# Kernel optimization log

Hardware: AMD Instinct MI355X
Metric: run time of the kernel (lower is better)

## Reference

```python
import jax, jax.numpy as jnp
import numpy as np

GRID_SIZE = 5
ORDER = 3  # spline_order
H_STEP = 2.0 / GRID_SIZE  # grid_range = [-1, 1]
GRID = jnp.arange(-ORDER, GRID_SIZE + ORDER + 1, dtype=jnp.float32) * H_STEP - 1.0  # (12,)


def b_splines(x):
    # x: (N, F) -> bases: (N, F, GRID_SIZE + ORDER) via Cox-de Boor recursion
    g = GRID
    xx = x[..., None]
    bases = ((xx >= g[:-1]) & (xx < g[1:])).astype(x.dtype)
    for k in range(1, ORDER + 1):
        left = (xx - g[:-(k + 1)]) / (g[k:-1] - g[:-(k + 1)]) * bases[..., :-1]
        right = (g[k + 1:] - xx) / (g[k + 1:] - g[1:-k]) * bases[..., 1:]
        bases = left + right
    return bases


def kan_linear(x, bw, sw, sc):
    # x: (N, F); bw: (O, F); sw: (O, F, C); sc: (O, F)
    base = jax.nn.silu(x) @ bw.T
    spline = jnp.einsum('nfc,ofc->no', b_splines(x), sw * sc[..., None])
    return base + spline


def kan_conv(x, bw, sw, sc):
    # x: (B, C, H, W); 3x3 patches, padding 1, stride 1 -> KANLinear over C*9 features
    B, C, H, W = x.shape
    patches = jax.lax.conv_general_dilated_patches(x, (3, 3), (1, 1), ((1, 1), (1, 1)))  # (B, C*9, H, W)
    p = patches.transpose(0, 2, 3, 1).reshape(B * H * W, C * 9)
    o = kan_linear(p, bw, sw, sc)  # (B*H*W, Cout)
    return o.reshape(B, H, W, -1).transpose(0, 3, 1, 2)


def maxpool2(x):
    B, C, H, W = x.shape
    return x.reshape(B, C, H // 2, 2, W // 2, 2).max(axis=(3, 5))


def setup_inputs() -> dict:
    key = jax.random.key(0)
    ks = jax.random.split(key, 32)
    d = {}
    d['x'] = jax.random.normal(ks[0], (128, 3, 32, 32), dtype=jnp.float32)
    conv_specs = [(3, 4), (4, 8), (8, 16), (16, 32)]
    i = 1
    for li, (cin, cout) in enumerate(conv_specs, 1):
        fin = cin * 9
        d[f'bw{li}'] = jax.random.normal(ks[i], (cout, fin), dtype=jnp.float32) * (1.0 / np.sqrt(fin)); i += 1
        d[f'sw{li}'] = jax.random.normal(ks[i], (cout, fin, GRID_SIZE + ORDER), dtype=jnp.float32) * 0.1; i += 1
        d[f'sc{li}'] = jax.random.normal(ks[i], (cout, fin), dtype=jnp.float32) * (1.0 / np.sqrt(fin)); i += 1
    lin_specs = [(2048, 2048), (1024, 2048), (10, 1024)]
    for li, (o, inn) in enumerate(lin_specs, 1):
        d[f'w{li}'] = jax.random.normal(ks[i], (o, inn), dtype=jnp.float32) * (1.0 / np.sqrt(inn)); i += 1
        d[f'b{li}'] = jnp.zeros((o,), dtype=jnp.float32); i += 1
    return d


def reference(x, bw1, sw1, sc1, bw2, sw2, sc2, bw3, sw3, sc3, bw4, sw4, sc4, w1, b1, w2, b2, w3, b3):
    x = kan_conv(x, bw1, sw1, sc1)
    x = kan_conv(x, bw2, sw2, sc2)
    x = maxpool2(x)
    x = kan_conv(x, bw3, sw3, sc3)
    x = kan_conv(x, bw4, sw4, sc4)
    x = maxpool2(x)
    x = x.reshape(x.shape[0], -1)  # (B, 32*8*8)
    x = jax.nn.relu(x @ w1.T + b1)
    x = jax.nn.relu(x @ w2.T + b2)
    return x @ w3.T + b3
```

## Files before the change

### kernel.cpp

```cpp
#include <hip/hip_runtime.h>

#define BATCH 128
#define AST 88

typedef __attribute__((ext_vector_type(8))) short bf16x8;
typedef __attribute__((ext_vector_type(16))) float f32x16;

__device__ __forceinline__ void spline_acts(float xv, float act[9]) {
    act[0] = xv * (1.0f / (1.0f + __expf(-xv)));
    float g[12];
#pragma unroll
    for (int i = 0; i < 12; ++i) g[i] = (float)(i - 3) * 0.4f - 1.0f;
    float bb[11];
#pragma unroll
    for (int c = 0; c < 11; ++c) bb[c] = (xv >= g[c] && xv < g[c + 1]) ? 1.0f : 0.0f;
#pragma unroll
    for (int k = 1; k <= 3; ++k) {
#pragma unroll
        for (int c = 0; c + k < 11; ++c) {
            float left  = (xv - g[c]) * (1.0f / (g[c + k] - g[c])) * bb[c];
            float right = (g[c + k + 1] - xv) * (1.0f / (g[c + k + 1] - g[c + 1])) * bb[c + 1];
            bb[c] = left + right;
        }
    }
#pragma unroll
    for (int c = 0; c < 8; ++c) act[c + 1] = bb[c];
}

__device__ __constant__ float ZPAD[9] = {0.0f, 0.0f, 0.0f, 0.02083333333f,
                                         0.47916666667f, 0.47916666667f,
                                         0.02083333333f, 0.0f, 0.0f};

__device__ __forceinline__ void bf16split(float x, ushort& h, ushort& l) {
    union { float f; unsigned u; } a; a.f = x;
    unsigned r = a.u + 0x7FFF + ((a.u >> 16) & 1);
    h = (ushort)(r >> 16);
    union { unsigned u; float f; } hf; hf.u = (unsigned)h << 16;
    union { float f; unsigned u; } bres; bres.f = x - hf.f;
    unsigned r2 = bres.u + 0x7FFF + ((bres.u >> 16) & 1);
    l = (ushort)(r2 >> 16);
}

__device__ __forceinline__ float wval(const float* bw, const float* sw, const float* sc,
                                      int F, int f, int j, int o) {
    if (j == 0) return bw[o * F + f];
    return sw[(o * F + f) * 8 + (j - 1)] * sc[o * F + f];
}

__global__ __launch_bounds__(256) void prep_kernel(
    const float* __restrict__ x,
    const float* __restrict__ bw1, const float* __restrict__ sw1, const float* __restrict__ sc1,
    const float* __restrict__ bw2, const float* __restrict__ sw2, const float* __restrict__ sc2,
    const float* __restrict__ bw3, const float* __restrict__ sw3, const float* __restrict__ sc3,
    const float* __restrict__ bw4, const float* __restrict__ sw4, const float* __restrict__ sc4,
    ushort* __restrict__ k1h, ushort* __restrict__ k1l,
    ushort* __restrict__ k2h, ushort* __restrict__ k2l,
    ushort* __restrict__ k3h, ushort* __restrict__ k3l,
    ushort* __restrict__ k4h, ushort* __restrict__ k4l,
    ushort* __restrict__ zph, ushort* __restrict__ zpl,
    ushort* __restrict__ A1h, ushort* __restrict__ A1l) {
    __shared__ unsigned SB[7168];
    if (blockIdx.x >= 46) {
        int bid = blockIdx.x - 46;
        int i = bid * 256 + threadIdx.x;
        int px = i & 1023, b = i >> 10;
        const float* xb = x + (size_t)b * 3072 + px;
        unsigned rh[14] = {}, rl[14] = {};
#pragma unroll
        for (int cin = 0; cin < 3; ++cin) {
            float a9[9];
            spline_acts(xb[cin * 1024], a9);
#pragma unroll
            for (int j = 0; j < 9; ++j) {
                ushort h, l2; bf16split(a9[j], h, l2);
                int c = cin * 9 + j;
                if (c & 1) { rh[c >> 1] |= (unsigned)h << 16; rl[c >> 1] |= (unsigned)l2 << 16; }
                else       { rh[c >> 1] |= h;                  rl[c >> 1] |= l2; }
            }
        }
        int wb = threadIdx.x * 14;
#pragma unroll
        for (int w = 0; w < 14; ++w) { SB[wb + w] = rh[w]; SB[3584 + wb + w] = rl[w]; }
        __syncthreads();
        const ushort* sb = (const ushort*)SB;
        size_t base = (size_t)bid * 7168;
#pragma unroll
        for (int e = 0; e < 4; ++e) {
            int q = e * 256 + threadIdx.x;
            if (q < 896) {
                *(uint4*)(A1h + base + q * 8) = *(const uint4*)(sb + q * 8);
                *(uint4*)(A1l + base + q * 8) = *(const uint4*)(sb + 7168 + q * 8);
            }
        }
        return;
    }
    int i = blockIdx.x * 256 + threadIdx.x;
    if (i < 1152) {
        int l = i & 63, s = (i >> 6) & 1, t = i / 128;
#pragma unroll
        for (int e = 0; e < 8; ++e) {
            int k = s * 16 + ((l >> 5) * 8) + e, o = l & 31;
            float w = 0.f;
            if (k < 27 && o < 4) w = wval(bw1, sw1, sc1, 27, (k / 9) * 9 + t, k % 9, o);
            ushort h, lo; bf16split(w, h, lo);
            k1h[i * 8 + e] = h; k1l[i * 8 + e] = lo;
        }
    } else if (i < 2880) {
        int q = i - 1152;
        int l = q & 63, s = (q >> 6) % 3, t = q / 192;
#pragma unroll
        for (int e = 0; e < 8; ++e) {
            int k = s * 16 + ((l >> 5) * 8) + e, o = l & 31;
            float w = 0.f;
            if (k < 36 && o < 8) w = wval(bw2, sw2, sc2, 36, (k / 9) * 9 + t, k % 9, o);
            ushort h, lo; bf16split(w, h, lo);
            k2h[q * 8 + e] = h; k2l[q * 8 + e] = lo;
        }
    } else if (i < 5760) {
        int q = i - 2880;
        int l = q & 63, s = (q >> 6) % 5, t = q / 320;
#pragma unroll
        for (int e = 0; e < 8; ++e) {
            int k = s * 16 + ((l >> 5) * 8) + e, o = l & 31;
            float w = 0.f;
            if (k < 72 && o < 16) w = wval(bw3, sw3, sc3, 72, (k / 9) * 9 + t, k % 9, o);
            ushort h, lo; bf16split(w, h, lo);
            k3h[q * 8 + e] = h; k3l[q * 8 + e] = lo;
        }
    } else if (i < 11520) {
        int q = i - 5760;
        int l = q & 63, s = (q >> 6) % 5, t = (q / 320) % 9, p = q / 2880;
#pragma unroll
        for (int e = 0; e < 8; ++e) {
            int k = s * 16 + ((l >> 5) * 8) + e, o = l & 31;
            float w = 0.f;
            if (k < 72) w = wval(bw4, sw4, sc4, 144, (p * 8 + k / 9) * 9 + t, k % 9, o);
            ushort h, lo; bf16split(w, h, lo);
            k4h[q * 8 + e] = h; k4l[q * 8 + e] = lo;
        }
    } else if (i < 11600) {
        int c = i - 11520;
        ushort h, lo; bf16split(ZPAD[c % 9], h, lo);
        zph[c] = h; zpl[c] = lo;
    }
}

template <int KG, int CHG, int CHL, int ASTR, int KSTEPS, int NCO, int EPI>
__global__ __launch_bounds__(256) void conv_strip(
    const ushort* __restrict__ Agh, const ushort* __restrict__ Agl,
    const ushort* __restrict__ Bgh, const ushort* __restrict__ Bgl,
    const ushort* __restrict__ zph, const ushort* __restrict__ zpl,
    ushort* __restrict__ Oh, ushort* __restrict__ Ol) {
    __shared__ ushort AH[340 * ASTR];
    __shared__ ushort AL[340 * ASTR];
    const int tid = threadIdx.x;
    const int b = blockIdx.x >> 2, strip = blockIdx.x & 3;
    const int r0 = strip * 8;
    const int lane = tid & 63, wv = tid >> 6;

    {
        const ushort* ash = Agh + (size_t)b * 1024 * KG;
        const ushort* asl = Agl + (size_t)b * 1024 * KG;
        for (int idx = tid; idx < 320 * CHL; idx += 256) {
            int pxl = idx / CHL, ch = idx - pxl * CHL;
            int lr = pxl >> 5, c = pxl & 31;
            int grow = r0 - 1 + lr;
            uint2 vh, vl;
            if (ch >= CHG) { vh = make_uint2(0u, 0u); vl = make_uint2(0u, 0u); }
            else if ((unsigned)grow < 32u) {
                vh = *(const uint2*)(ash + (size_t)(grow * 32 + c) * KG + ch * 4);
                vl = *(const uint2*)(asl + (size_t)(grow * 32 + c) * KG + ch * 4);
            } else {
                vh = *(const uint2*)(zph + ch * 4);
                vl = *(const uint2*)(zpl + ch * 4);
            }
            int spx = lr * 34 + c + 1;
            *(uint2*)(&AH[spx * ASTR + ch * 4]) = vh;
            *(uint2*)(&AL[spx * ASTR + ch * 4]) = vl;
        }
        for (int idx = tid; idx < 20 * CHL; idx += 256) {
            int sel = idx / CHL, ch = idx - sel * CHL;
            int lr = sel >> 1, c = (sel & 1) ? 33 : 0;
            int spx = lr * 34 + c;
            uint2 vh, vl;
            if (ch >= CHG) { vh = make_uint2(0u, 0u); vl = make_uint2(0u, 0u); }
            else { vh = *(const uint2*)(zph + ch * 4); vl = *(const uint2*)(zpl + ch * 4); }
            *(uint2*)(&AH[spx * ASTR + ch * 4]) = vh;
            *(uint2*)(&AL[spx * ASTR + ch * 4]) = vl;
        }
    }
    __syncthreads();

    f32x16 acc0, acc1;
#pragma unroll
    for (int i = 0; i < 16; ++i) { acc0[i] = 0.f; acc1[i] = 0.f; }

    const int p0 = wv * 64 + (lane & 31);
    const int sp0 = ((p0 >> 5) + 1) * 34 + (p0 & 31) + 1;
    const int sp1 = sp0 + 34;
    const int koff = (lane >> 5) * 8;

#pragma unroll 1
    for (int t = 0; t < 9; ++t) {
        const int dA = ((t / 3) - 1) * 34 + (t % 3) - 1;
#pragma unroll
        for (int s = 0; s < KSTEPS; ++s) {
            bf16x8 a0h = *(const bf16x8*)(&AH[(sp0 + dA) * ASTR + s * 16 + koff]);
            bf16x8 a0l = *(const bf16x8*)(&AL[(sp0 + dA) * ASTR + s * 16 + koff]);
            bf16x8 a1h = *(const bf16x8*)(&AH[(sp1 + dA) * ASTR + s * 16 + koff]);
            bf16x8 a1l = *(const bf16x8*)(&AL[(sp1 + dA) * ASTR + s * 16 + koff]);
            bf16x8 bh = *(const bf16x8*)(Bgh + (size_t)((t * KSTEPS + s) * 64 + lane) * 8);
            bf16x8 bl = *(const bf16x8*)(Bgl + (size_t)((t * KSTEPS + s) * 64 + lane) * 8);
            acc0 = __builtin_amdgcn_mfma_f32_32x32x16_bf16(a0h, bh, acc0, 0, 0, 0);
            acc1 = __builtin_amdgcn_mfma_f32_32x32x16_bf16(a1h, bh, acc1, 0, 0, 0);
            acc0 = __builtin_amdgcn_mfma_f32_32x32x16_bf16(a0h, bl, acc0, 0, 0, 0);
            acc1 = __builtin_amdgcn_mfma_f32_32x32x16_bf16(a1h, bl, acc1, 0, 0, 0);
            acc0 = __builtin_amdgcn_mfma_f32_32x32x16_bf16(a0l, bh, acc0, 0, 0, 0);
            acc1 = __builtin_amdgcn_mfma_f32_32x32x16_bf16(a1l, bh, acc1, 0, 0, 0);
        }
    }
    __syncthreads();

    float* fl = (float*)AH;
    {
        int ccol = lane & 31;
        if (ccol < NCO) {
#pragma unroll
            for (int r = 0; r < 16; ++r) {
                int row = (r & 3) + 8 * (r >> 2) + 4 * (lane >> 5);
                fl[ccol * 257 + wv * 64 + row] = acc0[r];
                fl[ccol * 257 + wv * 64 + 32 + row] = acc1[r];
            }
        }
    }
    __syncthreads();

    if (EPI == 0) {
        unsigned* ubh = (unsigned*)AL;
        unsigned* ubl = (unsigned*)AH + 1032;
        unsigned rwh[18], rwl[18];
#pragma unroll
        for (int w = 0; w < 18; ++w) { rwh[w] = 0u; rwl[w] = 0u; }
#pragma unroll
        for (int co = 0; co < 4; ++co) {
            float a9[9];
            spline_acts(fl[co * 257 + tid], a9);
#pragma unroll
            for (int j = 0; j < 9; ++j) {
                ushort h, l2; bf16split(a9[j], h, l2);
                int c = co * 9 + j;
                if (c & 1) { rwh[c >> 1] |= (unsigned)h << 16; rwl[c >> 1] |= (unsigned)l2 << 16; }
                else       { rwh[c >> 1] |= h;                  rwl[c >> 1] |= l2; }
            }
        }
#pragma unroll
        for (int w = 0; w < 18; ++w) { ubh[tid * 18 + w] = rwh[w]; ubl[tid * 18 + w] = rwl[w]; }
        __syncthreads();
        size_t basew = ((size_t)b * 1024 + strip * 256) * 18;
        unsigned* goh = (unsigned*)Oh + basew;
        unsigned* gol = (unsigned*)Ol + basew;
#pragma unroll
        for (int e = 0; e < 18; ++e) {
            int q = e * 256 + tid;
            goh[q] = ubh[q];
            gol[q] = ubl[q];
        }
    } else {
        int cg = tid >> 6, pl = tid & 63;
        int phl = pl >> 4, pw = pl & 15;
        int base_m = (2 * phl) * 32 + 2 * pw;
        unsigned rwh[9], rwl[9];
#pragma unroll
        for (int w = 0; w < 9; ++w) { rwh[w] = 0u; rwl[w] = 0u; }
#pragma unroll
        for (int e = 0; e < 2; ++e) {
            int co = cg * 2 + e;
            const float* fb = fl + co * 257 + base_m;
            float m = fmaxf(fmaxf(fb[0], fb[1]), fmaxf(fb[32], fb[33]));
            float a9[9];
            spline_acts(m, a9);
#pragma unroll
            for (int j = 0; j < 9; ++j) {
                ushort h, l2; bf16split(a9[j], h, l2);
                int c = e * 9 + j;
                if (c & 1) { rwh[c >> 1] |= (unsigned)h << 16; rwl[c >> 1] |= (unsigned)l2 << 16; }
                else       { rwh[c >> 1] |= h;                  rwl[c >> 1] |= l2; }
            }
        }
        unsigned* ubh = (unsigned*)AL;
        unsigned* ubl = (unsigned*)AL + 2560;
#pragma unroll
        for (int w = 0; w < 9; ++w) {
            ubh[pl * 40 + cg * 9 + w] = rwh[w];
            ubl[pl * 40 + cg * 9 + w] = rwl[w];
        }
        if (cg == 3) {
#pragma unroll
            for (int w = 0; w < 4; ++w) { ubh[pl * 40 + 36 + w] = 0u; ubl[pl * 40 + 36 + w] = 0u; }
        }
        __syncthreads();
        size_t base = ((size_t)b * 256 + strip * 64) * 80;
        const ushort* sbh = (const ushort*)ubh;
        const ushort* sbl = (const ushort*)ubl;
#pragma unroll
        for (int e = 0; e < 3; ++e) {
            int q = e * 256 + tid;
            if (q < 640) {
                *(uint4*)(Oh + base + q * 8) = *(const uint4*)(sbh + q * 8);
                *(uint4*)(Ol + base + q * 8) = *(const uint4*)(sbl + q * 8);
            }
        }
    }
}

template <int NPH, int NCO>
__global__ __launch_bounds__(256) void conv34_part(
    const ushort* __restrict__ Agh, const ushort* __restrict__ Agl,
    const ushort* __restrict__ Bgh, const ushort* __restrict__ Bgl,
    const ushort* __restrict__ zph, const ushort* __restrict__ zpl,
    float* __restrict__ P) {
    __shared__ ushort AH[144 * AST];
    __shared__ ushort AL[144 * AST];
    const int tid = threadIdx.x;
    const int b = blockIdx.x, half = blockIdx.y, g = blockIdx.z;
    const int r0 = half * 8;
    const int lane = tid & 63, wv = tid >> 6;

    f32x16 acc;
#pragma unroll
    for (int i = 0; i < 16; ++i) acc[i] = 0.f;

    const int m = wv * 32 + (lane & 31);
    const int sbase = (m >> 4) * 18 + (m & 15);
    const int koff = (lane >> 5) * 8;

#pragma unroll 1
    for (int p = 0; p < NPH; ++p) {
        if (p) __syncthreads();
        const ushort* ash = Agh + ((size_t)b * NPH + p) * 256 * 80;
        const ushort* asl = Agl + ((size_t)b * NPH + p) * 256 * 80;
#pragma unroll
        for (int e = 0; e < 6; ++e) {
            int idx = e * 256 + tid;
            if (idx < 1440) {
                int px = idx / 10, ch = idx - px * 10;
                int pr = px / 18, pc = px - pr * 18;
                int r = r0 - 1 + g + pr, c = pc - 1;
                bool inb = ((unsigned)r < 16u) && ((unsigned)c < 16u);
                uint4 vh, vl;
                if (inb) {
                    vh = *(const uint4*)(ash + (size_t)(r * 16 + c) * 80 + ch * 8);
                    vl = *(const uint4*)(asl + (size_t)(r * 16 + c) * 80 + ch * 8);
                } else {
                    vh = *(const uint4*)(zph + ch * 8);
                    vl = *(const uint4*)(zpl + ch * 8);
                }
                *(uint4*)(&AH[px * AST + ch * 8]) = vh;
                *(uint4*)(&AL[px * AST + ch * 8]) = vl;
            }
        }
        __syncthreads();

        const ushort* bsh = Bgh + (size_t)p * 2880 * 8;
        const ushort* bsl = Bgl + (size_t)p * 2880 * 8;
#pragma unroll
        for (int dw = 0; dw < 3; ++dw) {
            const int t = g * 3 + dw;
#pragma unroll
            for (int s = 0; s < 5; ++s) {
                bf16x8 ah = *(const bf16x8*)(&AH[(sbase + dw) * AST + s * 16 + koff]);
                bf16x8 al = *(const bf16x8*)(&AL[(sbase + dw) * AST + s * 16 + koff]);
                bf16x8 bh = *(const bf16x8*)(bsh + (size_t)((t * 5 + s) * 64 + lane) * 8);
                bf16x8 bl = *(const bf16x8*)(bsl + (size_t)((t * 5 + s) * 64 + lane) * 8);
                acc = __builtin_amdgcn_mfma_f32_32x32x16_bf16(ah, bh, acc, 0, 0, 0);
                acc = __builtin_amdgcn_mfma_f32_32x32x16_bf16(ah, bl, acc, 0, 0, 0);
                acc = __builtin_amdgcn_mfma_f32_32x32x16_bf16(al, bh, acc, 0, 0, 0);
            }
        }
    }

    int co = lane & 31;
    if (co < NCO) {
        float* pb = P + ((size_t)(g * 256 + b * 2 + half) * 128) * NCO;
#pragma unroll
        for (int r = 0; r < 16; ++r) {
            int px = wv * 32 + (r & 3) + 8 * (r >> 2) + 4 * (lane >> 5);
            pb[px * NCO + co] = acc[r];
        }
    }
}

__global__ __launch_bounds__(256) void conv3_reduce(const float* __restrict__ P3,
                                                    ushort* __restrict__ A4h,
                                                    ushort* __restrict__ A4l) {
    __shared__ ushort SBH[2][64 * 80];
    __shared__ ushort SBL[2][64 * 80];
    int b = blockIdx.x, pxq = blockIdx.y;
    int t = threadIdx.x;
    int co = t & 15, pxg = t >> 4;
#pragma unroll
    for (int q = 0; q < 4; ++q) {
        int lpx64 = pxg * 4 + q;
        int px = pxq * 64 + lpx64;
        int bh = b * 2 + (px >> 7), lpx = px & 127;
        float s = 0.f;
#pragma unroll
        for (int zz = 0; zz < 3; ++zz)
            s += P3[((size_t)(zz * 256 + bh) * 128 + lpx) * 16 + co];
        float a9[9];
        spline_acts(s, a9);
        int ph = co >> 3, c8 = co & 7;
#pragma unroll
        for (int j = 0; j < 9; ++j) {
            ushort h, l2; bf16split(a9[j], h, l2);
            SBH[ph][lpx64 * 80 + c8 * 9 + j] = h;
            SBL[ph][lpx64 * 80 + c8 * 9 + j] = l2;
        }
        if (c8 == 7) {
#pragma unroll
            for (int w = 0; w < 8; ++w) {
                SBH[ph][lpx64 * 80 + 72 + w] = 0;
                SBL[ph][lpx64 * 80 + 72 + w] = 0;
            }
        }
    }
    __syncthreads();
#pragma unroll
    for (int ph = 0; ph < 2; ++ph) {
        size_t base = ((size_t)(b * 2 + ph) * 256 + pxq * 64) * 80;
#pragma unroll
        for (int e = 0; e < 3; ++e) {
            int q = e * 256 + t;
            if (q < 640) {
                *(uint4*)(A4h + base + q * 8) = *(const uint4*)(&SBH[ph][q * 8]);
                *(uint4*)(A4l + base + q * 8) = *(const uint4*)(&SBL[ph][q * 8]);
            }
        }
    }
}

__global__ __launch_bounds__(256) void conv4_reduce_pool(const float* __restrict__ P4,
                                                         float* __restrict__ pooled) {
    __shared__ float SM[32 * 33];
    int b = blockIdx.x, half = blockIdx.y;
    int t = threadIdx.x;
    int co = t & 31, pg = t >> 5;
    int bh = b * 2 + half;
#pragma unroll
    for (int q = 0; q < 4; ++q) {
        int pp = pg * 4 + q;
        int lr = pp >> 3, pc = pp & 7;
        int px00 = (2 * lr) * 16 + 2 * pc;
        float s00 = 0.f, s01 = 0.f, s10 = 0.f, s11 = 0.f;
#pragma unroll
        for (int zz = 0; zz < 3; ++zz) {
            const float* pb = P4 + ((size_t)(zz * 256 + bh) * 128) * 32 + co;
            s00 += pb[(size_t)px00 * 32];
            s01 += pb[(size_t)(px00 + 1) * 32];
            s10 += pb[(size_t)(px00 + 16) * 32];
            s11 += pb[(size_t)(px00 + 17) * 32];
        }
        SM[co * 33 + pp] = fmaxf(fmaxf(s00, s01), fmaxf(s10, s11));
    }
    __syncthreads();
#pragma unroll
    for (int e = 0; e < 4; ++e) {
        int idx = e * 256 + t;
        int co2 = idx >> 5, pp2 = idx & 31;
        int lr2 = pp2 >> 3, pc2 = pp2 & 7;
        pooled[(size_t)b * 2048 + co2 * 64 + (half * 4 + lr2) * 8 + pc2] = SM[co2 * 33 + pp2];
    }
}

template <int SPLIT>
__global__ __launch_bounds__(256) void fc_big(const float* __restrict__ A,
                                              const float* __restrict__ Wt,
                                              float* __restrict__ part,
                                              int M, int N, int K) {
    __shared__ float As[32][68];
    __shared__ float Ws[32][68];
    const int tid = threadIdx.x;
    const int tx = tid & 15, ty = tid >> 4;
    const int bm = blockIdx.y * 64, bn = blockIdx.x * 64;
    const int kc = K / SPLIT;
    const int kbeg = blockIdx.z * kc;
    float acc[4][4] = {};
    for (int k0 = kbeg; k0 < kbeg + kc; k0 += 32) {
#pragma unroll
        for (int e = 0; e < 2; ++e) {
            int q = e * 256 + tid;
            int r = q >> 3, k4 = (q & 7) * 4;
            float4 av = *(const float4*)&A[(size_t)(bm + r) * K + k0 + k4];
            float4 wv = *(const float4*)&Wt[(size_t)(bn + r) * K + k0 + k4];
            As[k4 + 0][r] = av.x; As[k4 + 1][r] = av.y;
            As[k4 + 2][r] = av.z; As[k4 + 3][r] = av.w;
            Ws[k4 + 0][r] = wv.x; Ws[k4 + 1][r] = wv.y;
            Ws[k4 + 2][r] = wv.z; Ws[k4 + 3][r] = wv.w;
        }
        __syncthreads();
#pragma unroll
        for (int kk = 0; kk < 32; ++kk) {
            float4 av = *(const float4*)(&As[kk][ty * 4]);
            float4 wv = *(const float4*)(&Ws[kk][tx * 4]);
            acc[0][0] = fmaf(av.x, wv.x, acc[0][0]);
            acc[0][1] = fmaf(av.x, wv.y, acc[0][1]);
            acc[0][2] = fmaf(av.x, wv.z, acc[0][2]);
            acc[0][3] = fmaf(av.x, wv.w, acc[0][3]);
            acc[1][0] = fmaf(av.y, wv.x, acc[1][0]);
            acc[1][1] = fmaf(av.y, wv.y, acc[1][1]);
            acc[1][2] = fmaf(av.y, wv.z, acc[1][2]);
            acc[1][3] = fmaf(av.y, wv.w, acc[1][3]);
            acc[2][0] = fmaf(av.z, wv.x, acc[2][0]);
            acc[2][1] = fmaf(av.z, wv.y, acc[2][1]);
            acc[2][2] = fmaf(av.z, wv.z, acc[2][2]);
            acc[2][3] = fmaf(av.z, wv.w, acc[2][3]);
            acc[3][0] = fmaf(av.w, wv.x, acc[3][0]);
            acc[3][1] = fmaf(av.w, wv.y, acc[3][1]);
            acc[3][2] = fmaf(av.w, wv.z, acc[3][2]);
            acc[3][3] = fmaf(av.w, wv.w, acc[3][3]);
        }
        __syncthreads();
    }
    float* p = part + (size_t)blockIdx.z * M * N;
#pragma unroll
    for (int i = 0; i < 4; ++i) {
        float4 v = make_float4(acc[i][0], acc[i][1], acc[i][2], acc[i][3]);
        *(float4*)&p[(size_t)(bm + ty * 4 + i) * N + (bn + tx * 4)] = v;
    }
}

template <int SPLIT>
__global__ void fc_reduce(const float* __restrict__ part, const float* __restrict__ bias,
                          float* __restrict__ C, int MN, int N, int relu) {
    int i = blockIdx.x * 256 + threadIdx.x;
    if (i >= MN) return;
    float s = bias[i % N];
#pragma unroll
    for (int z = 0; z < SPLIT; ++z) s += part[(size_t)z * MN + i];
    C[i] = relu ? fmaxf(s, 0.f) : s;
}

__global__ __launch_bounds__(256) void fc3_kernel(const float* __restrict__ A,
                                                  const float* __restrict__ Wt,
                                                  const float* __restrict__ bias,
                                                  float* __restrict__ C) {
    int gid = blockIdx.x * 256 + threadIdx.x;
    int wid = gid >> 6;
    int lane = gid & 63;
    int m = wid / 10, n = wid - m * 10;
    const float4* a = (const float4*)(A + (size_t)m * 1024);
    const float4* w = (const float4*)(Wt + (size_t)n * 1024);
    float s = 0.f;
#pragma unroll
    for (int it = 0; it < 4; ++it) {
        float4 av = a[it * 64 + lane];
        float4 wv = w[it * 64 + lane];
        s += av.x * wv.x + av.y * wv.y + av.z * wv.z + av.w * wv.w;
    }
#pragma unroll
    for (int off = 32; off; off >>= 1) s += __shfl_xor(s, off);
    if (lane == 0) C[wid] = s + bias[n];
}

extern "C" void kernel_launch(void* const* d_in, const int* in_sizes, int n_in,
                              void* d_out, int out_size, void* d_ws, size_t ws_size,
                              hipStream_t stream) {
    const float* x   = (const float*)d_in[0];
    const float* bw1 = (const float*)d_in[1];
    const float* sw1 = (const float*)d_in[2];
    const float* sc1 = (const float*)d_in[3];
    const float* bw2 = (const float*)d_in[4];
    const float* sw2 = (const float*)d_in[5];
    const float* sc2 = (const float*)d_in[6];
    const float* bw3 = (const float*)d_in[7];
    const float* sw3 = (const float*)d_in[8];
    const float* sc3 = (const float*)d_in[9];
    const float* bw4 = (const float*)d_in[10];
    const float* sw4 = (const float*)d_in[11];
    const float* sc4 = (const float*)d_in[12];
    const float* w1  = (const float*)d_in[13];
    const float* b1  = (const float*)d_in[14];
    const float* w2  = (const float*)d_in[15];
    const float* b2  = (const float*)d_in[16];
    const float* w3  = (const float*)d_in[17];
    const float* b3  = (const float*)d_in[18];

    float*  wsf = (float*)d_ws;
    ushort* wsu = (ushort*)d_ws;
    ushort* k1h = wsu + 110848;
    ushort* k1l = wsu + 120064;
    ushort* k2h = wsu + 129280;
    ushort* k2l = wsu + 143104;
    ushort* k3h = wsu + 156928;
    ushort* k3l = wsu + 179968;
    ushort* k4h = wsu + 203008;
    ushort* k4l = wsu + 249088;
    ushort* zph = wsu + 295168;
    ushort* zpl = wsu + 295248;
    ushort* A1h = wsu + 524288;
    ushort* A1l = wsu + 4194304;
    ushort* A2h = wsu + 7864320;
    ushort* A2l = wsu + 12582912;
    ushort* A3h = wsu + 524288;
    ushort* A3l = wsu + 3145728;
    ushort* A4h = wsu + 5767168;
    ushort* A4l = wsu + 11010048;
    float* P3   = wsf + 9437184;
    float* P4   = wsf + 11534336;
    float* pooled = wsf + 262144;
    float* part1  = wsf + 524288;
    float* fc1o   = wsf + 2621440;
    float* part2  = wsf + 2883584;
    float* fc2o   = wsf + 3932160;

    prep_kernel<<<558, 256, 0, stream>>>(x, bw1, sw1, sc1, bw2, sw2, sc2,
                                         bw3, sw3, sc3, bw4, sw4, sc4,
                                         k1h, k1l, k2h, k2l, k3h, k3l, k4h, k4l,
                                         zph, zpl, A1h, A1l);

    conv_strip<28, 7, 8, 40, 2, 4, 0><<<512, 256, 0, stream>>>(A1h, A1l, k1h, k1l,
                                                               zph, zpl, A2h, A2l);
    conv_strip<36, 9, 12, 56, 3, 8, 1><<<512, 256, 0, stream>>>(A2h, A2l, k2h, k2l,
                                                                zph, zpl, A3h, A3l);
    conv34_part<1, 16><<<dim3(128, 2, 3), 256, 0, stream>>>(A3h, A3l, k3h, k3l,
                                                            zph, zpl, P3);
    conv3_reduce<<<dim3(128, 4), 256, 0, stream>>>(P3, A4h, A4l);
    conv34_part<2, 32><<<dim3(128, 2, 3), 256, 0, stream>>>(A4h, A4l, k4h, k4l,
                                                            zph, zpl, P4);
    conv4_reduce_pool<<<dim3(128, 2), 256, 0, stream>>>(P4, pooled);

    fc_big<8><<<dim3(32, 2, 8), 256, 0, stream>>>(pooled, w1, part1, 128, 2048, 2048);
    fc_reduce<8><<<1024, 256, 0, stream>>>(part1, b1, fc1o, 262144, 2048, 1);
    fc_big<8><<<dim3(16, 2, 8), 256, 0, stream>>>(fc1o, w2, part2, 128, 1024, 2048);
    fc_reduce<8><<<512, 256, 0, stream>>>(part2, b2, fc2o, 131072, 1024, 1);
    fc3_kernel<<<320, 256, 0, stream>>>(fc2o, w3, b3, (float*)d_out);
}
```

Before: 136.8 us.

## Fuse first-layer spline activation computation into conv1 strip kernel

Result: faster. 132.0 us (-3.5%).

```diff
diff --git a/kernel.cpp b/kernel.cpp
--- a/kernel.cpp
+++ b/kernel.cpp
@@ -48,7 +48,6 @@
 }
 
 __global__ __launch_bounds__(256) void prep_kernel(
-    const float* __restrict__ x,
     const float* __restrict__ bw1, const float* __restrict__ sw1, const float* __restrict__ sc1,
     const float* __restrict__ bw2, const float* __restrict__ sw2, const float* __restrict__ sc2,
     const float* __restrict__ bw3, const float* __restrict__ sw3, const float* __restrict__ sc3,
@@ -57,43 +56,7 @@
     ushort* __restrict__ k2h, ushort* __restrict__ k2l,
     ushort* __restrict__ k3h, ushort* __restrict__ k3l,
     ushort* __restrict__ k4h, ushort* __restrict__ k4l,
-    ushort* __restrict__ zph, ushort* __restrict__ zpl,
-    ushort* __restrict__ A1h, ushort* __restrict__ A1l) {
-    __shared__ unsigned SB[7168];
-    if (blockIdx.x >= 46) {
-        int bid = blockIdx.x - 46;
-        int i = bid * 256 + threadIdx.x;
-        int px = i & 1023, b = i >> 10;
-        const float* xb = x + (size_t)b * 3072 + px;
-        unsigned rh[14] = {}, rl[14] = {};
-#pragma unroll
-        for (int cin = 0; cin < 3; ++cin) {
-            float a9[9];
-            spline_acts(xb[cin * 1024], a9);
-#pragma unroll
-            for (int j = 0; j < 9; ++j) {
-                ushort h, l2; bf16split(a9[j], h, l2);
-                int c = cin * 9 + j;
-                if (c & 1) { rh[c >> 1] |= (unsigned)h << 16; rl[c >> 1] |= (unsigned)l2 << 16; }
-                else       { rh[c >> 1] |= h;                  rl[c >> 1] |= l2; }
-            }
-        }
-        int wb = threadIdx.x * 14;
-#pragma unroll
-        for (int w = 0; w < 14; ++w) { SB[wb + w] = rh[w]; SB[3584 + wb + w] = rl[w]; }
-        __syncthreads();
-        const ushort* sb = (const ushort*)SB;
-        size_t base = (size_t)bid * 7168;
-#pragma unroll
-        for (int e = 0; e < 4; ++e) {
-            int q = e * 256 + threadIdx.x;
-            if (q < 896) {
-                *(uint4*)(A1h + base + q * 8) = *(const uint4*)(sb + q * 8);
-                *(uint4*)(A1l + base + q * 8) = *(const uint4*)(sb + 7168 + q * 8);
-            }
-        }
-        return;
-    }
+    ushort* __restrict__ zph, ushort* __restrict__ zpl) {
     int i = blockIdx.x * 256 + threadIdx.x;
     if (i < 1152) {
         int l = i & 63, s = (i >> 6) & 1, t = i / 128;
@@ -145,8 +108,131 @@
     }
 }
 
-template <int KG, int CHG, int CHL, int ASTR, int KSTEPS, int NCO, int EPI>
-__global__ __launch_bounds__(256) void conv_strip(
+__global__ __launch_bounds__(256) void conv1_fused(
+    const float* __restrict__ x,
+    const ushort* __restrict__ Bgh, const ushort* __restrict__ Bgl,
+    ushort* __restrict__ Oh, ushort* __restrict__ Ol) {
+    constexpr int ASTR = 40, KSTEPS = 2, NCO = 4;
+    __shared__ ushort AH[340 * ASTR];
+    __shared__ ushort AL[340 * ASTR];
+    const int tid = threadIdx.x;
+    const int b = blockIdx.x >> 2, strip = blockIdx.x & 3;
+    const int r0 = strip * 8;
+    const int lane = tid & 63, wv = tid >> 6;
+
+    for (int px = tid; px < 340; px += 256) {
+        int lr = px / 34, pc = px - lr * 34;
+        int grow = r0 - 1 + lr, gc = pc - 1;
+        bool inb = ((unsigned)grow < 32u) && ((unsigned)gc < 32u);
+        unsigned rh[16], rl[16];
+#pragma unroll
+        for (int w = 0; w < 16; ++w) { rh[w] = 0u; rl[w] = 0u; }
+        if (inb) {
+            const float* xb = x + (size_t)b * 3072 + grow * 32 + gc;
+#pragma unroll
+            for (int cin = 0; cin < 3; ++cin) {
+                float a9[9];
+                spline_acts(xb[cin * 1024], a9);
+#pragma unroll
+                for (int j = 0; j < 9; ++j) {
+                    ushort h, l2; bf16split(a9[j], h, l2);
+                    int c = cin * 9 + j;
+                    if (c & 1) { rh[c >> 1] |= (unsigned)h << 16; rl[c >> 1] |= (unsigned)l2 << 16; }
+                    else       { rh[c >> 1] |= h;                  rl[c >> 1] |= l2; }
+                }
+            }
+        } else {
+#pragma unroll
+            for (int c = 0; c < 27; ++c) {
+                ushort h, l2; bf16split(ZPAD[c % 9], h, l2);
+                if (c & 1) { rh[c >> 1] |= (unsigned)h << 16; rl[c >> 1] |= (unsigned)l2 << 16; }
+                else       { rh[c >> 1] |= h;                  rl[c >> 1] |= l2; }
+            }
+        }
+        unsigned* dh = (unsigned*)&AH[px * ASTR];
+        unsigned* dl = (unsigned*)&AL[px * ASTR];
+#pragma unroll
+        for (int w = 0; w < 16; ++w) { dh[w] = rh[w]; dl[w] = rl[w]; }
+    }
+    __syncthreads();
+
+    f32x16 acc0, acc1;
+#pragma unroll
+    for (int i = 0; i < 16; ++i) { acc0[i] = 0.f; acc1[i] = 0.f; }
+
+    const int p0 = wv * 64 + (lane & 31);
+    const int sp0 = ((p0 >> 5) + 1) * 34 + (p0 & 31) + 1;
+    const int sp1 = sp0 + 34;
+    const int koff = (lane >> 5) * 8;
+
+#pragma unroll 1
+    for (int t = 0; t < 9; ++t) {
+        const int dA = ((t / 3) - 1) * 34 + (t % 3) - 1;
+#pragma unroll
+        for (int s = 0; s < KSTEPS; ++s) {
+            bf16x8 a0h = *(const bf16x8*)(&AH[(sp0 + dA) * ASTR + s * 16 + koff]);
+            bf16x8 a0l = *(const bf16x8*)(&AL[(sp0 + dA) * ASTR + s * 16 + koff]);
+            bf16x8 a1h = *(const bf16x8*)(&AH[(sp1 + dA) * ASTR + s * 16 + koff]);
+            bf16x8 a1l = *(const bf16x8*)(&AL[(sp1 + dA) * ASTR + s * 16 + koff]);
+            bf16x8 bh = *(const bf16x8*)(Bgh + (size_t)((t * KSTEPS + s) * 64 + lane) * 8);
+            bf16x8 bl = *(const bf16x8*)(Bgl + (size_t)((t * KSTEPS + s) * 64 + lane) * 8);
+            acc0 = __builtin_amdgcn_mfma_f32_32x32x16_bf16(a0h, bh, acc0, 0, 0, 0);
+            acc1 = __builtin_amdgcn_mfma_f32_32x32x16_bf16(a1h, bh, acc1, 0, 0, 0);
+            acc0 = __builtin_amdgcn_mfma_f32_32x32x16_bf16(a0h, bl, acc0, 0, 0, 0);
+            acc1 = __builtin_amdgcn_mfma_f32_32x32x16_bf16(a1h, bl, acc1, 0, 0, 0);
+            acc0 = __builtin_amdgcn_mfma_f32_32x32x16_bf16(a0l, bh, acc0, 0, 0, 0);
+            acc1 = __builtin_amdgcn_mfma_f32_32x32x16_bf16(a1l, bh, acc1, 0, 0, 0);
+        }
+    }
+    __syncthreads();
+
+    float* fl = (float*)AH;
+    {
+        int ccol = lane & 31;
+        if (ccol < NCO) {
+#pragma unroll
+            for (int r = 0; r < 16; ++r) {
+                int row = (r & 3) + 8 * (r >> 2) + 4 * (lane >> 5);
+                fl[ccol * 257 + wv * 64 + row] = acc0[r];
+                fl[ccol * 257 + wv * 64 + 32 + row] = acc1[r];
+            }
+        }
+    }
+    __syncthreads();
+
+    unsigned* ubh = (unsigned*)AL;
+    unsigned* ubl = (unsigned*)AH + 1032;
+    unsigned rwh[18], rwl[18];
+#pragma unroll
+    for (int w = 0; w < 18; ++w) { rwh[w] = 0u; rwl[w] = 0u; }
+#pragma unroll
+    for (int co = 0; co < 4; ++co) {
+        float a9[9];
+        spline_acts(fl[co * 257 + tid], a9);
+#pragma unroll
+        for (int j = 0; j < 9; ++j) {
+            ushort h, l2; bf16split(a9[j], h, l2);
+            int c = co * 9 + j;
+            if (c & 1) { rwh[c >> 1] |= (unsigned)h << 16; rwl[c >> 1] |= (unsigned)l2 << 16; }
+            else       { rwh[c >> 1] |= h;                  rwl[c >> 1] |= l2; }
+        }
+    }
+#pragma unroll
+    for (int w = 0; w < 18; ++w) { ubh[tid * 18 + w] = rwh[w]; ubl[tid * 18 + w] = rwl[w]; }
+    __syncthreads();
+    size_t basew = ((size_t)b * 1024 + strip * 256) * 18;
+    unsigned* goh = (unsigned*)Oh + basew;
+    unsigned* gol = (unsigned*)Ol + basew;
+#pragma unroll
+    for (int e = 0; e < 18; ++e) {
+        int q = e * 256 + tid;
+        goh[q] = ubh[q];
+        gol[q] = ubl[q];
+    }
+}
+
+template <int KG, int CHG, int CHL, int ASTR, int KSTEPS, int NCO>
+__global__ __launch_bounds__(256) void conv2_strip(
     const ushort* __restrict__ Agh, const ushort* __restrict__ Agl,
     const ushort* __restrict__ Bgh, const ushort* __restrict__ Bgl,
     const ushort* __restrict__ zph, const ushort* __restrict__ zpl,
@@ -235,80 +321,48 @@
     }
     __syncthreads();
 
-    if (EPI == 0) {
-        unsigned* ubh = (unsigned*)AL;
-        unsigned* ubl = (unsigned*)AH + 1032;
-        unsigned rwh[18], rwl[18];
-#pragma unroll
-        for (int w = 0; w < 18; ++w) { rwh[w] = 0u; rwl[w] = 0u; }
-#pragma unroll
-        for (int co = 0; co < 4; ++co) {
-            float a9[9];
-            spline_acts(fl[co * 257 + tid], a9);
-#pragma unroll
-            for (int j = 0; j < 9; ++j) {
-                ushort h, l2; bf16split(a9[j], h, l2);
-                int c = co * 9 + j;
-                if (c & 1) { rwh[c >> 1] |= (unsigned)h << 16; rwl[c >> 1] |= (unsigned)l2 << 16; }
-                else       { rwh[c >> 1] |= h;                  rwl[c >> 1] |= l2; }
-            }
-        }
-#pragma unroll
-        for (int w = 0; w < 18; ++w) { ubh[tid * 18 + w] = rwh[w]; ubl[tid * 18 + w] = rwl[w]; }
-        __syncthreads();
-        size_t basew = ((size_t)b * 1024 + strip * 256) * 18;
-        unsigned* goh = (unsigned*)Oh + basew;
-        unsigned* gol = (unsigned*)Ol + basew;
-#pragma unroll
-        for (int e = 0; e < 18; ++e) {
-            int q = e * 256 + tid;
-            goh[q] = ubh[q];
-            gol[q] = ubl[q];
-        }
-    } else {
-        int cg = tid >> 6, pl = tid & 63;
-        int phl = pl >> 4, pw = pl & 15;
-        int base_m = (2 * phl) * 32 + 2 * pw;
-        unsigned rwh[9], rwl[9];
-#pragma unroll
-        for (int w = 0; w < 9; ++w) { rwh[w] = 0u; rwl[w] = 0u; }
-#pragma unroll
-        for (int e = 0; e < 2; ++e) {
-            int co = cg * 2 + e;
-            const float* fb = fl + co * 257 + base_m;
-            float m = fmaxf(fmaxf(fb[0], fb[1]), fmaxf(fb[32], fb[33]));
-            float a9[9];
-            spline_acts(m, a9);
-#pragma unroll
-            for (int j = 0; j < 9; ++j) {
-                ushort h, l2; bf16split(a9[j], h, l2);
-                int c = e * 9 + j;
-                if (c & 1) { rwh[c >> 1] |= (unsigned)h << 16; rwl[c >> 1] |= (unsigned)l2 << 16; }
-                else       { rwh[c >> 1] |= h;                  rwl[c >> 1] |= l2; }
-            }
-        }
-        unsigned* ubh = (unsigned*)AL;
-        unsigned* ubl = (unsigned*)AL + 2560;
-#pragma unroll
-        for (int w = 0; w < 9; ++w) {
-            ubh[pl * 40 + cg * 9 + w] = rwh[w];
-            ubl[pl * 40 + cg * 9 + w] = rwl[w];
-        }
-        if (cg == 3) {
-#pragma unroll
-            for (int w = 0; w < 4; ++w) { ubh[pl * 40 + 36 + w] = 0u; ubl[pl * 40 + 36 + w] = 0u; }
-        }
-        __syncthreads();
-        size_t base = ((size_t)b * 256 + strip * 64) * 80;
-        const ushort* sbh = (const ushort*)ubh;
-        const ushort* sbl = (const ushort*)ubl;
-#pragma unroll
-        for (int e = 0; e < 3; ++e) {
-            int q = e * 256 + tid;
-            if (q < 640) {
-                *(uint4*)(Oh + base + q * 8) = *(const uint4*)(sbh + q * 8);
-                *(uint4*)(Ol + base + q * 8) = *(const uint4*)(sbl + q * 8);
-            }
+    int cg = tid >> 6, pl = tid & 63;
+    int phl = pl >> 4, pw = pl & 15;
+    int base_m = (2 * phl) * 32 + 2 * pw;
+    unsigned rwh[9], rwl[9];
+#pragma unroll
+    for (int w = 0; w < 9; ++w) { rwh[w] = 0u; rwl[w] = 0u; }
+#pragma unroll
+    for (int e = 0; e < 2; ++e) {
+        int co = cg * 2 + e;
+        const float* fb = fl + co * 257 + base_m;
+        float m = fmaxf(fmaxf(fb[0], fb[1]), fmaxf(fb[32], fb[33]));
+        float a9[9];
+        spline_acts(m, a9);
+#pragma unroll
+        for (int j = 0; j < 9; ++j) {
+            ushort h, l2; bf16split(a9[j], h, l2);
+            int c = e * 9 + j;
+            if (c & 1) { rwh[c >> 1] |= (unsigned)h << 16; rwl[c >> 1] |= (unsigned)l2 << 16; }
+            else       { rwh[c >> 1] |= h;                  rwl[c >> 1] |= l2; }
+        }
+    }
+    unsigned* ubh = (unsigned*)AL;
+    unsigned* ubl = (unsigned*)AL + 2560;
+#pragma unroll
+    for (int w = 0; w < 9; ++w) {
+        ubh[pl * 40 + cg * 9 + w] = rwh[w];
+        ubl[pl * 40 + cg * 9 + w] = rwl[w];
+    }
+    if (cg == 3) {
+#pragma unroll
+        for (int w = 0; w < 4; ++w) { ubh[pl * 40 + 36 + w] = 0u; ubl[pl * 40 + 36 + w] = 0u; }
+    }
+    __syncthreads();
+    size_t base = ((size_t)b * 256 + strip * 64) * 80;
+    const ushort* sbh = (const ushort*)ubh;
+    const ushort* sbl = (const ushort*)ubl;
+#pragma unroll
+    for (int e = 0; e < 3; ++e) {
+        int q = e * 256 + tid;
+        if (q < 640) {
+            *(uint4*)(Oh + base + q * 8) = *(const uint4*)(sbh + q * 8);
+            *(uint4*)(Ol + base + q * 8) = *(const uint4*)(sbl + q * 8);
         }
     }
 }
@@ -597,8 +651,6 @@
     ushort* k4l = wsu + 249088;
     ushort* zph = wsu + 295168;
     ushort* zpl = wsu + 295248;
-    ushort* A1h = wsu + 524288;
-    ushort* A1l = wsu + 4194304;
     ushort* A2h = wsu + 7864320;
     ushort* A2l = wsu + 12582912;
     ushort* A3h = wsu + 524288;
@@ -613,15 +665,14 @@
     float* part2  = wsf + 2883584;
     float* fc2o   = wsf + 3932160;
 
-    prep_kernel<<<558, 256, 0, stream>>>(x, bw1, sw1, sc1, bw2, sw2, sc2,
-                                         bw3, sw3, sc3, bw4, sw4, sc4,
-                                         k1h, k1l, k2h, k2l, k3h, k3l, k4h, k4l,
-                                         zph, zpl, A1h, A1l);
-
-    conv_strip<28, 7, 8, 40, 2, 4, 0><<<512, 256, 0, stream>>>(A1h, A1l, k1h, k1l,
-                                                               zph, zpl, A2h, A2l);
-    conv_strip<36, 9, 12, 56, 3, 8, 1><<<512, 256, 0, stream>>>(A2h, A2l, k2h, k2l,
-                                                                zph, zpl, A3h, A3l);
+    prep_kernel<<<46, 256, 0, stream>>>(bw1, sw1, sc1, bw2, sw2, sc2,
+                                        bw3, sw3, sc3, bw4, sw4, sc4,
+                                        k1h, k1l, k2h, k2l, k3h, k3l, k4h, k4l,
+                                        zph, zpl);
+
+    conv1_fused<<<512, 256, 0, stream>>>(x, k1h, k1l, A2h, A2l);
+    conv2_strip<36, 9, 12, 56, 3, 8><<<512, 256, 0, stream>>>(A2h, A2l, k2h, k2l,
+                                                              zph, zpl, A3h, A3l);
     conv34_part<1, 16><<<dim3(128, 2, 3), 256, 0, stream>>>(A3h, A3l, k3h, k3l,
                                                             zph, zpl, P3);
     conv3_reduce<<<dim3(128, 4), 256, 0, stream>>>(P3, A4h, A4l);
```
